# Performance work log

Hardware: AMD Instinct MI355X
Metric: run time of the kernel (lower is better)

## Reference

```python
import jax, jax.numpy as jnp
import numpy as np

N_HEAD = 8
LN_EPS = 1e-5


def _ln(x, g, b):
    m = jnp.mean(x, axis=-1, keepdims=True)
    v = jnp.mean((x - m) ** 2, axis=-1, keepdims=True)
    return (x - m) * jax.lax.rsqrt(v + LN_EPS) * g + b


def setup_inputs() -> dict:
    B, S, IN, D, F, OUT, L = 4, 2048, 3, 512, 2048, 20, 6
    key = jax.random.key(0)
    ks = jax.random.split(key, 22)
    sc = 0.02
    return {
        'src': jax.random.normal(ks[0], (B, S, IN), jnp.float32),
        'W_in': jax.random.normal(ks[1], (IN, D), jnp.float32) * sc,
        'b_in': jnp.zeros((D,), jnp.float32),
        'Wq': jax.random.normal(ks[2], (L, D, D), jnp.float32) * sc,
        'bq': jnp.zeros((L, D), jnp.float32),
        'Wk': jax.random.normal(ks[3], (L, D, D), jnp.float32) * sc,
        'bk': jnp.zeros((L, D), jnp.float32),
        'Wv': jax.random.normal(ks[4], (L, D, D), jnp.float32) * sc,
        'bv': jnp.zeros((L, D), jnp.float32),
        'Wo': jax.random.normal(ks[5], (L, D, D), jnp.float32) * sc,
        'bo': jnp.zeros((L, D), jnp.float32),
        'ln1_g': jnp.ones((L, D), jnp.float32),
        'ln1_b': jnp.zeros((L, D), jnp.float32),
        'W1': jax.random.normal(ks[6], (L, D, F), jnp.float32) * sc,
        'b1': jnp.zeros((L, F), jnp.float32),
        'W2': jax.random.normal(ks[7], (L, F, D), jnp.float32) * sc,
        'b2': jnp.zeros((L, D), jnp.float32),
        'ln2_g': jnp.ones((L, D), jnp.float32),
        'ln2_b': jnp.zeros((L, D), jnp.float32),
        'W_out': jax.random.normal(ks[8], (D, OUT), jnp.float32) * sc,
        'b_out': jnp.zeros((OUT,), jnp.float32),
    }


def reference(src, W_in, b_in, Wq, bq, Wk, bk, Wv, bv, Wo, bo, ln1_g, ln1_b,
              W1, b1, W2, b2, ln2_g, ln2_b, W_out, b_out):
    x = src @ W_in + b_in            # [B, S, D]
    B, S, D = x.shape
    dh = D // N_HEAD
    scale = 1.0 / np.sqrt(dh).astype(np.float32)

    def layer(x, p):
        wq, biq, wk, bik, wv, biv, wo, bio, g1, be1, w1, bi1, w2, bi2, g2, be2 = p
        q = (x @ wq + biq).reshape(B, S, N_HEAD, dh)
        k = (x @ wk + bik).reshape(B, S, N_HEAD, dh)
        v = (x @ wv + biv).reshape(B, S, N_HEAD, dh)
        # flex_attention with score_mod=None == plain scaled dot-product attention
        scores = jnp.einsum('bqhd,bkhd->bhqk', q, k) * scale
        a = jax.nn.softmax(scores, axis=-1)
        o = jnp.einsum('bhqk,bkhd->bqhd', a, v).reshape(B, S, D)
        attn = o @ wo + bio
        h = _ln(x + attn, g1, be1)                       # post-norm (norm_first=False)
        ff = jax.nn.relu(h @ w1 + bi1) @ w2 + bi2
        h = _ln(h + ff, g2, be2)
        return h, None

    x, _ = jax.lax.scan(layer, x, (Wq, bq, Wk, bk, Wv, bv, Wo, bo,
                                   ln1_g, ln1_b, W1, b1, W2, b2, ln2_g, ln2_b))
    return x @ W_out + b_out         # [B, S, OUT]
```

## Files before the change

kernel.cpp:

```cpp
#include <hip/hip_runtime.h>

typedef unsigned short u16;
typedef unsigned int u32;
typedef __bf16 bf16x8 __attribute__((ext_vector_type(8)));
typedef float f32x4 __attribute__((ext_vector_type(4)));
typedef float f32x16 __attribute__((ext_vector_type(16)));

__device__ __forceinline__ u16 f2bf(float f) {
    union { float f; u32 u; } v; v.f = f;
    u32 r = v.u + 0x7FFFu + ((v.u >> 16) & 1u);
    return (u16)(r >> 16);
}

__device__ __forceinline__ u16 bfu(float x) {
    __bf16 b = (__bf16)x;
    union { __bf16 b; u16 u; } c; c.b = b; return c.u;
}

__device__ __forceinline__ void gload16(const u16* g, u16* l) {
    __builtin_amdgcn_global_load_lds((const __attribute__((address_space(1))) void*)g,
                                     (__attribute__((address_space(3))) void*)l, 16, 0, 0);
}

__global__ void wtrans(const float* __restrict__ W, u16* __restrict__ Wt,
                       int K, int N, int rowOff, int dstLd, long long dstStride)
{
    __shared__ float tile[32][33];
    const int l = blockIdx.z;
    const float* Wl = W + (size_t)l * K * N;
    u16* Wtl = Wt + (size_t)l * dstStride;
    const int tx = threadIdx.x, ty = threadIdx.y;
    const int x = blockIdx.x * 32 + tx;
    const int y0 = blockIdx.y * 32;
#pragma unroll
    for (int j = 0; j < 32; j += 8) tile[ty + j][tx] = Wl[(size_t)(y0 + ty + j) * N + x];
    __syncthreads();
    const int n0 = blockIdx.x * 32;
    const int k = y0 + tx;
#pragma unroll
    for (int j = 0; j < 32; j += 8)
        Wtl[(size_t)(rowOff + n0 + ty + j) * dstLd + k] = f2bf(tile[tx][ty + j]);
}

__global__ __launch_bounds__(256) void input_proj(const float* __restrict__ src,
    const float* __restrict__ Wi, const float* __restrict__ bi,
    float* __restrict__ xf, u16* __restrict__ xb)
{
    int idx = blockIdx.x * 256 + threadIdx.x;
    int m = idx >> 9, n = idx & 511;
    float v = bi[n] + src[m * 3] * Wi[n] + src[m * 3 + 1] * Wi[512 + n] + src[m * 3 + 2] * Wi[1024 + n];
    xf[idx] = v;
    xb[idx] = f2bf(v);
}

template<int EPI>
__global__ __launch_bounds__(256) void gemm_bt(
    const u16* __restrict__ A, const u16* __restrict__ Bt,
    const float* __restrict__ bias,
    float* __restrict__ Cf, u16* __restrict__ Cb,
    u16* __restrict__ Qo, u16* __restrict__ Ko, u16* __restrict__ Vo,
    const float* __restrict__ bq, const float* __restrict__ bk, const float* __restrict__ bv,
    int M, int N, int K)
{
    __shared__ u16 As[128 * 32];
    __shared__ u16 Bs[128 * 32];
    const int tid = threadIdx.x;
    const int lane = tid & 63, wid = tid >> 6;
    const int bn = blockIdx.x, bm = blockIdx.y;
    const int row0 = bm * 128, col0 = bn * 128;
    const int srow = lane >> 2, skc = lane & 3;
    const int c0 = wid * 2, c1 = wid * 2 + 1;
    const u16* gA0 = A + (size_t)(row0 + c0 * 16 + srow) * K + skc * 8;
    const u16* gA1 = A + (size_t)(row0 + c1 * 16 + srow) * K + skc * 8;
    const u16* gB0 = Bt + (size_t)(col0 + c0 * 16 + srow) * K + skc * 8;
    const u16* gB1 = Bt + (size_t)(col0 + c1 * 16 + srow) * K + skc * 8;
    u16* lA0 = &As[c0 * 512]; u16* lA1 = &As[c1 * 512];
    u16* lB0 = &Bs[c0 * 512]; u16* lB1 = &Bs[c1 * 512];
    const int wr = (wid >> 1) * 64, wc = (wid & 1) * 64;
    const int cc = lane & 15, qg = lane >> 4;
    const int arow0 = (wr + cc) * 32 + qg * 8;
    const int brow0 = (wc + cc) * 32 + qg * 8;
    f32x4 acc[4][4] = {};
    for (int k0 = 0; k0 < K; k0 += 32) {
        __syncthreads();
        gload16(gA0 + k0, lA0);
        gload16(gA1 + k0, lA1);
        gload16(gB0 + k0, lB0);
        gload16(gB1 + k0, lB1);
        __syncthreads();
        bf16x8 af[4], bfr[4];
#pragma unroll
        for (int i = 0; i < 4; i++) af[i] = *(const bf16x8*)&As[arow0 + i * 512];
#pragma unroll
        for (int i = 0; i < 4; i++) bfr[i] = *(const bf16x8*)&Bs[brow0 + i * 512];
#pragma unroll
        for (int mi = 0; mi < 4; mi++)
#pragma unroll
            for (int ni = 0; ni < 4; ni++)
                acc[mi][ni] = __builtin_amdgcn_mfma_f32_16x16x32_bf16(af[mi], bfr[ni], acc[mi][ni], 0, 0, 0);
    }
    const int q4 = qg * 4;
    if (EPI == 2) {
#pragma unroll
        for (int mi = 0; mi < 4; mi++) {
            int grow = row0 + wr + mi * 16 + q4;
            int btok = grow >> 11, srem = grow & 2047;
#pragma unroll
            for (int ni = 0; ni < 4; ni++) {
                int gcol = col0 + wc + ni * 16 + cc;
                int sec = gcol >> 9, f = gcol & 511;
                int hh = f >> 6, dd = f & 63;
                if (sec == 0) {
                    float bb = bq[f];
                    size_t base = (((size_t)btok * 8 + hh) * 2048 + srem) * 64 + dd;
#pragma unroll
                    for (int i = 0; i < 4; i++) Qo[base + (size_t)i * 64] = f2bf((acc[mi][ni][i] + bb) * 0.18033688f);
                } else if (sec == 1) {
                    float bb = bk[f];
                    size_t base = (((size_t)btok * 8 + hh) * 2048 + srem) * 64 + dd;
#pragma unroll
                    for (int i = 0; i < 4; i++) Ko[base + (size_t)i * 64] = f2bf(acc[mi][ni][i] + bb);
                } else {
                    float bb = bv[f];
                    size_t base = (((size_t)btok * 8 + hh) * 64 + dd) * 2048 + srem;
#pragma unroll
                    for (int i = 0; i < 4; i++) Vo[base + i] = f2bf(acc[mi][ni][i] + bb);
                }
            }
        }
    } else {
#pragma unroll
        for (int mi = 0; mi < 4; mi++) {
            int grow = row0 + wr + mi * 16 + q4;
#pragma unroll
            for (int ni = 0; ni < 4; ni++) {
                int gcol = col0 + wc + ni * 16 + cc;
                float bb = bias[gcol];
#pragma unroll
                for (int i = 0; i < 4; i++) {
                    float v = acc[mi][ni][i] + bb;
                    if (EPI == 0) Cf[(size_t)(grow + i) * N + gcol] = v;
                    else          Cb[(size_t)(grow + i) * N + gcol] = f2bf(v > 0.f ? v : 0.f);
                }
            }
        }
    }
}

__global__ __launch_bounds__(256) void gemm_bt_n64(
    const u16* __restrict__ A, const u16* __restrict__ Bt,
    const float* __restrict__ bias, float* __restrict__ Cf,
    int M, int N, int K)
{
    __shared__ u16 As[128 * 64];
    __shared__ u16 Bs[64 * 64];
    const int tid = threadIdx.x;
    const int lane = tid & 63, wid = tid >> 6;
    const int row0 = blockIdx.y * 128, col0 = blockIdx.x * 64;
    const int wr = (wid >> 1) * 64, wc = (wid & 1) * 32;
    const int cc = lane & 15, qg = lane >> 4;
    f32x4 acc[4][2] = {};
    for (int k0 = 0; k0 < K; k0 += 64) {
        __syncthreads();
#pragma unroll
        for (int j = 0; j < 4; j++) {
            int s = j * 256 + tid;
            int r = s >> 3, g = s & 7;
            gload16(A + (size_t)(row0 + r) * K + k0 + (g ^ (r & 7)) * 8, &As[s * 8]);
        }
#pragma unroll
        for (int j = 0; j < 2; j++) {
            int s = j * 256 + tid;
            int r = s >> 3, g = s & 7;
            gload16(Bt + (size_t)(col0 + r) * K + k0 + (g ^ (r & 7)) * 8, &Bs[s * 8]);
        }
        __syncthreads();
        bf16x8 af[4][2], bfr[2][2];
#pragma unroll
        for (int i = 0; i < 4; i++) {
            int r = wr + i * 16 + cc;
#pragma unroll
            for (int kk = 0; kk < 2; kk++) {
                int g = kk * 4 + qg;
                af[i][kk] = *(const bf16x8*)&As[r * 64 + (g ^ (r & 7)) * 8];
            }
        }
#pragma unroll
        for (int i = 0; i < 2; i++) {
            int r = wc + i * 16 + cc;
#pragma unroll
            for (int kk = 0; kk < 2; kk++) {
                int g = kk * 4 + qg;
                bfr[i][kk] = *(const bf16x8*)&Bs[r * 64 + (g ^ (r & 7)) * 8];
            }
        }
#pragma unroll
        for (int mi = 0; mi < 4; mi++)
#pragma unroll
            for (int ni = 0; ni < 2; ni++) {
                acc[mi][ni] = __builtin_amdgcn_mfma_f32_16x16x32_bf16(af[mi][0], bfr[ni][0], acc[mi][ni], 0, 0, 0);
                acc[mi][ni] = __builtin_amdgcn_mfma_f32_16x16x32_bf16(af[mi][1], bfr[ni][1], acc[mi][ni], 0, 0, 0);
            }
    }
    const int q4 = qg * 4;
#pragma unroll
    for (int mi = 0; mi < 4; mi++) {
        int grow = row0 + wr + mi * 16 + q4;
#pragma unroll
        for (int ni = 0; ni < 2; ni++) {
            int gcol = col0 + wc + ni * 16 + cc;
            float bb = bias[gcol];
#pragma unroll
            for (int i = 0; i < 4; i++)
                Cf[(size_t)(grow + i) * N + gcol] = acc[mi][ni][i] + bb;
        }
    }
}

__global__ __launch_bounds__(128) void flash_attn(
    const u16* __restrict__ Qb, const u16* __restrict__ Kb, const u16* __restrict__ Vt,
    u16* __restrict__ Ob)
{
    __shared__ u16 Ks[2][4096];
    __shared__ u16 Vs[2][4096];
    const int tid = threadIdx.x, lane = tid & 63, w = tid >> 6;
    const int l31 = lane & 31, h = lane >> 5;
    const int bh = blockIdx.x, qt = blockIdx.y;
    const u16* Kg = Kb + (size_t)bh * (2048 * 64);
    const u16* Vg = Vt + (size_t)bh * (64 * 2048);

    bf16x8 qf[4];
    {
        const u16* Qrow = Qb + ((size_t)bh * 2048 + (size_t)qt * 64 + w * 32 + l31) * 64;
#pragma unroll
        for (int f = 0; f < 4; f++) qf[f] = *(const bf16x8*)(Qrow + f * 16 + h * 8);
    }
    f32x16 os0{}, os1{};
    float lsum = 0.f;

    const int sr = tid >> 3, sg = tid & 7;
#pragma unroll
    for (int j = 0; j < 4; j++) {
        int r = j * 16 + sr;
        int gsw = (sg ^ (r & 7)) * 8;
        gload16(Kg + (size_t)r * 64 + gsw, &Ks[0][(j * 128 + w * 64) * 8]);
        gload16(Vg + (size_t)r * 2048 + gsw, &Vs[0][(j * 128 + w * 64) * 8]);
    }
    const int swz = (l31 & 7) << 3;

    for (int kt = 0; kt < 32; kt++) {
        const int cur = kt & 1;
        asm volatile("s_waitcnt vmcnt(0)" ::: "memory");
        __syncthreads();
        if (kt < 31) {
#pragma unroll
            for (int j = 0; j < 4; j++) {
                int r = j * 16 + sr;
                int gsw = (sg ^ (r & 7)) * 8;
                gload16(Kg + (size_t)(kt + 1) * 4096 + (size_t)r * 64 + gsw, &Ks[cur ^ 1][(j * 128 + w * 64) * 8]);
                gload16(Vg + (size_t)r * 2048 + (size_t)(kt + 1) * 64 + gsw, &Vs[cur ^ 1][(j * 128 + w * 64) * 8]);
            }
        }
        f32x16 p0{}, p1{};
        {
            const u16* kb = &Ks[cur][0];
            __builtin_amdgcn_s_setprio(1);
#pragma unroll
            for (int f = 0; f < 4; f++) {
                int colu = (f * 16 + h * 8) ^ swz;
                bf16x8 ka0 = *(const bf16x8*)(kb + l31 * 64 + colu);
                bf16x8 ka1 = *(const bf16x8*)(kb + (32 + l31) * 64 + colu);
                p0 = __builtin_amdgcn_mfma_f32_32x32x16_bf16(ka0, qf[f], p0, 0, 0, 0);
                p1 = __builtin_amdgcn_mfma_f32_32x32x16_bf16(ka1, qf[f], p1, 0, 0, 0);
            }
            __builtin_amdgcn_s_setprio(0);
        }
        float ss[4] = {};
#pragma unroll
        for (int r = 0; r < 16; r++) { float e = __builtin_amdgcn_exp2f(p0[r]); p0[r] = e; ss[r & 3] += e; }
#pragma unroll
        for (int r = 0; r < 16; r++) { float e = __builtin_amdgcn_exp2f(p1[r]); p1[r] = e; ss[r & 3] += e; }
        lsum += (ss[0] + ss[1]) + (ss[2] + ss[3]);
        const u16* vb = &Vs[cur][0];
#pragma unroll
        for (int t = 0; t < 2; t++) {
            u32 pk[8], sw[8];
#pragma unroll
            for (int j = 0; j < 8; j++) {
                float a = t ? p1[2 * j] : p0[2 * j];
                float b = t ? p1[2 * j + 1] : p0[2 * j + 1];
                pk[j] = (u32)bfu(a) | ((u32)bfu(b) << 16);
                sw[j] = __shfl_xor(pk[j], 32);
            }
            union { u32 u[4]; bf16x8 v; } fA, fB;
            fA.u[0] = h ? sw[2] : pk[0];
            fA.u[1] = h ? sw[3] : pk[1];
            fA.u[2] = h ? pk[2] : sw[0];
            fA.u[3] = h ? pk[3] : sw[1];
            fB.u[0] = h ? sw[6] : pk[4];
            fB.u[1] = h ? sw[7] : pk[5];
            fB.u[2] = h ? pk[6] : sw[4];
            fB.u[3] = h ? pk[7] : sw[5];
            __builtin_amdgcn_s_setprio(1);
#pragma unroll
            for (int f = 0; f < 2; f++) {
                bf16x8 pa = f ? fB.v : fA.v;
                int colu = (t * 32 + f * 16 + h * 8) ^ swz;
                bf16x8 v0 = *(const bf16x8*)(vb + l31 * 64 + colu);
                bf16x8 v1 = *(const bf16x8*)(vb + (32 + l31) * 64 + colu);
                os0 = __builtin_amdgcn_mfma_f32_32x32x16_bf16(pa, v0, os0, 0, 0, 0);
                os1 = __builtin_amdgcn_mfma_f32_32x32x16_bf16(pa, v1, os1, 0, 0, 0);
            }
            __builtin_amdgcn_s_setprio(0);
        }
    }
    lsum += __shfl_xor(lsum, 32);
    float rl = 1.f / lsum;
    const int hatt = bh & 7, b_ = bh >> 3;
#pragma unroll
    for (int r = 0; r < 16; r++) {
        int qrow = (r & 3) + 8 * (r >> 2) + 4 * h;
        float rlq = __shfl(rl, qrow);
        int tok = qt * 64 + w * 32 + qrow;
        u16* po = Ob + ((size_t)b_ * 2048 + tok) * 512 + hatt * 64;
        po[l31] = bfu(os0[r] * rlq);
        po[32 + l31] = bfu(os1[r] * rlq);
    }
}

__global__ __launch_bounds__(256) void ln_res(
    const float* __restrict__ X, const float* __restrict__ Y,
    const float* __restrict__ g, const float* __restrict__ bta,
    float* __restrict__ Of, u16* __restrict__ Ob)
{
    const int lane = threadIdx.x & 63;
    const int row = blockIdx.x * 4 + (threadIdx.x >> 6);
    const size_t base = (size_t)row * 512 + lane * 8;
    float4 x0 = *(const float4*)(X + base);
    float4 x1 = *(const float4*)(X + base + 4);
    float4 y0 = *(const float4*)(Y + base);
    float4 y1 = *(const float4*)(Y + base + 4);
    float t[8] = {x0.x + y0.x, x0.y + y0.y, x0.z + y0.z, x0.w + y0.w,
                  x1.x + y1.x, x1.y + y1.y, x1.z + y1.z, x1.w + y1.w};
    float s = 0.f, s2 = 0.f;
#pragma unroll
    for (int j = 0; j < 8; j++) { s += t[j]; s2 += t[j] * t[j]; }
#pragma unroll
    for (int off = 1; off < 64; off <<= 1) { s += __shfl_xor(s, off); s2 += __shfl_xor(s2, off); }
    float mean = s * (1.f / 512.f);
    float var = s2 * (1.f / 512.f) - mean * mean;
    float rs = rsqrtf(var + 1e-5f);
    float4 g0 = *(const float4*)(g + lane * 8);
    float4 g1 = *(const float4*)(g + lane * 8 + 4);
    float4 b0 = *(const float4*)(bta + lane * 8);
    float4 b1 = *(const float4*)(bta + lane * 8 + 4);
    float gg[8] = {g0.x, g0.y, g0.z, g0.w, g1.x, g1.y, g1.z, g1.w};
    float bb[8] = {b0.x, b0.y, b0.z, b0.w, b1.x, b1.y, b1.z, b1.w};
    float o[8];
#pragma unroll
    for (int j = 0; j < 8; j++) o[j] = (t[j] - mean) * rs * gg[j] + bb[j];
    *(float4*)(Of + base) = make_float4(o[0], o[1], o[2], o[3]);
    *(float4*)(Of + base + 4) = make_float4(o[4], o[5], o[6], o[7]);
    u32 p0 = (u32)f2bf(o[0]) | ((u32)f2bf(o[1]) << 16);
    u32 p1 = (u32)f2bf(o[2]) | ((u32)f2bf(o[3]) << 16);
    u32 p2 = (u32)f2bf(o[4]) | ((u32)f2bf(o[5]) << 16);
    u32 p3 = (u32)f2bf(o[6]) | ((u32)f2bf(o[7]) << 16);
    *(uint4*)(Ob + base) = make_uint4(p0, p1, p2, p3);
}

__global__ __launch_bounds__(320) void out_proj(const float* __restrict__ x,
    const float* __restrict__ W, const float* __restrict__ b, float* __restrict__ out)
{
    int t = blockIdx.x * 320 + threadIdx.x;
    int m = t / 20, o = t - m * 20;
    const float* xr = x + (size_t)m * 512;
    float acc = b[o];
#pragma unroll 8
    for (int k = 0; k < 512; k++) acc = fmaf(xr[k], W[k * 20 + o], acc);
    out[(size_t)m * 20 + o] = acc;
}

extern "C" void kernel_launch(void* const* d_in, const int* in_sizes, int n_in,
                              void* d_out, int out_size, void* d_ws, size_t ws_size,
                              hipStream_t stream)
{
    const float* src  = (const float*)d_in[0];
    const float* W_in = (const float*)d_in[1];
    const float* b_in = (const float*)d_in[2];
    const float* Wq   = (const float*)d_in[3];
    const float* bq   = (const float*)d_in[4];
    const float* Wk   = (const float*)d_in[5];
    const float* bk   = (const float*)d_in[6];
    const float* Wv   = (const float*)d_in[7];
    const float* bv   = (const float*)d_in[8];
    const float* Wo   = (const float*)d_in[9];
    const float* bo   = (const float*)d_in[10];
    const float* ln1g = (const float*)d_in[11];
    const float* ln1b = (const float*)d_in[12];
    const float* W1   = (const float*)d_in[13];
    const float* b1   = (const float*)d_in[14];
    const float* W2   = (const float*)d_in[15];
    const float* b2   = (const float*)d_in[16];
    const float* ln2g = (const float*)d_in[17];
    const float* ln2b = (const float*)d_in[18];
    const float* Wout = (const float*)d_in[19];
    const float* bout = (const float*)d_in[20];

    char* ws = (char*)d_ws;
    size_t off = 0;
    auto take = [&](size_t bytes) -> void* {
        off = (off + 255) & ~(size_t)255;
        void* p = ws + off;
        off += bytes;
        return p;
    };
    const size_t TOK = 8192, D = 512;
    u16*   qkvt = (u16*)take(6ull * 1536 * 512 * 2);
    u16*   wot  = (u16*)take(6ull * 512 * 512 * 2);
    u16*   w1t  = (u16*)take(6ull * 2048 * 512 * 2);
    u16*   w2t  = (u16*)take(6ull * 512 * 2048 * 2);
    float* xf   = (float*)take(TOK * D * 4);
    u16*   xb   = (u16*)take(TOK * D * 2);
    u16*   sh4  = (u16*)take(4ull * TOK * D * 2);
    float* scr  = (float*)take(TOK * D * 4);
    float* h1f  = (float*)take(TOK * D * 4);
    u16*   h1b  = (u16*)take(TOK * D * 2);
    if (off > ws_size) return;

    u16* qb  = sh4;
    u16* kb_ = sh4 + TOK * D;
    u16* vtb = sh4 + 2 * TOK * D;
    u16* ob  = sh4 + 3 * TOK * D;
    u16* ffb = sh4;

    dim3 tb(32, 8);
    wtrans<<<dim3(16, 16, 6), tb, 0, stream>>>(Wq, qkvt, 512, 512, 0,    512, 1536ll * 512);
    wtrans<<<dim3(16, 16, 6), tb, 0, stream>>>(Wk, qkvt, 512, 512, 512,  512, 1536ll * 512);
    wtrans<<<dim3(16, 16, 6), tb, 0, stream>>>(Wv, qkvt, 512, 512, 1024, 512, 1536ll * 512);
    wtrans<<<dim3(16, 16, 6), tb, 0, stream>>>(Wo, wot,  512, 512, 0,    512, 512ll * 512);
    wtrans<<<dim3(64, 16, 6), tb, 0, stream>>>(W1, w1t,  512, 2048, 0,   512, 2048ll * 512);
    wtrans<<<dim3(16, 64, 6), tb, 0, stream>>>(W2, w2t,  2048, 512, 0,  2048, 512ll * 2048);

    input_proj<<<16384, 256, 0, stream>>>(src, W_in, b_in, xf, xb);

    for (int l = 0; l < 6; l++) {
        const u16* qkvt_l = qkvt + (size_t)l * 1536 * 512;
        const u16* wot_l  = wot  + (size_t)l * 512 * 512;
        const u16* w1t_l  = w1t  + (size_t)l * 2048 * 512;
        const u16* w2t_l  = w2t  + (size_t)l * 512 * 2048;

        gemm_bt<2><<<dim3(12, 64), 256, 0, stream>>>(xb, qkvt_l, nullptr,
            nullptr, nullptr, qb, kb_, vtb,
            bq + l * 512, bk + l * 512, bv + l * 512, 8192, 1536, 512);

        flash_attn<<<dim3(32, 32), 128, 0, stream>>>(qb, kb_, vtb, ob);

        gemm_bt_n64<<<dim3(8, 64), 256, 0, stream>>>(ob, wot_l, bo + l * 512,
            scr, 8192, 512, 512);

        ln_res<<<2048, 256, 0, stream>>>(xf, scr, ln1g + l * 512, ln1b + l * 512, h1f, h1b);

        gemm_bt<1><<<dim3(16, 64), 256, 0, stream>>>(h1b, w1t_l, b1 + l * 2048,
            nullptr, ffb, nullptr, nullptr, nullptr, nullptr, nullptr, nullptr,
            8192, 2048, 512);

        gemm_bt_n64<<<dim3(8, 64), 256, 0, stream>>>(ffb, w2t_l, b2 + l * 512,
            scr, 8192, 512, 2048);

        ln_res<<<2048, 256, 0, stream>>>(h1f, scr, ln2g + l * 512, ln2b + l * 512, xf, xb);
    }

    out_proj<<<512, 320, 0, stream>>>(xf, Wout, bout, (float*)d_out);
}
```

Measured before the change: 1.222 ms.

## Double GEMM K-tile with swizzled LDS and widen flash-attn blocks to 128 queries

The gemm_bt kernel now loads 64-wide K tiles into LDS with an XOR swizzle and issues two MFMAs per fragment per iteration. This halves the number of barrier pairs and reduces LDS bank conflicts. Flash attention now runs 4 waves per block covering 128 query rows, so each K/V tile loaded into LDS is reused by twice as many queries. In exchange it uses more LDS per GEMM block and launches half as many attention blocks, which may lower occupancy.

```diff
diff --git a/kernel.cpp b/kernel.cpp
--- a/kernel.cpp
+++ b/kernel.cpp
@@ -62,42 +62,52 @@
     const float* __restrict__ bq, const float* __restrict__ bk, const float* __restrict__ bv,
     int M, int N, int K)
 {
-    __shared__ u16 As[128 * 32];
-    __shared__ u16 Bs[128 * 32];
+    __shared__ u16 As[128 * 64];
+    __shared__ u16 Bs[128 * 64];
     const int tid = threadIdx.x;
     const int lane = tid & 63, wid = tid >> 6;
-    const int bn = blockIdx.x, bm = blockIdx.y;
-    const int row0 = bm * 128, col0 = bn * 128;
-    const int srow = lane >> 2, skc = lane & 3;
-    const int c0 = wid * 2, c1 = wid * 2 + 1;
-    const u16* gA0 = A + (size_t)(row0 + c0 * 16 + srow) * K + skc * 8;
-    const u16* gA1 = A + (size_t)(row0 + c1 * 16 + srow) * K + skc * 8;
-    const u16* gB0 = Bt + (size_t)(col0 + c0 * 16 + srow) * K + skc * 8;
-    const u16* gB1 = Bt + (size_t)(col0 + c1 * 16 + srow) * K + skc * 8;
-    u16* lA0 = &As[c0 * 512]; u16* lA1 = &As[c1 * 512];
-    u16* lB0 = &Bs[c0 * 512]; u16* lB1 = &Bs[c1 * 512];
+    const int row0 = blockIdx.y * 128, col0 = blockIdx.x * 128;
     const int wr = (wid >> 1) * 64, wc = (wid & 1) * 64;
     const int cc = lane & 15, qg = lane >> 4;
-    const int arow0 = (wr + cc) * 32 + qg * 8;
-    const int brow0 = (wc + cc) * 32 + qg * 8;
+    const int sr = tid >> 3, sg = tid & 7;
     f32x4 acc[4][4] = {};
-    for (int k0 = 0; k0 < K; k0 += 32) {
+    for (int k0 = 0; k0 < K; k0 += 64) {
         __syncthreads();
-        gload16(gA0 + k0, lA0);
-        gload16(gA1 + k0, lA1);
-        gload16(gB0 + k0, lB0);
-        gload16(gB1 + k0, lB1);
+#pragma unroll
+        for (int j = 0; j < 4; j++) {
+            int r = j * 32 + sr;
+            int gsw = (sg ^ (r & 7)) * 8;
+            gload16(A + (size_t)(row0 + r) * K + k0 + gsw, &As[(j * 256 + tid) * 8]);
+        }
+#pragma unroll
+        for (int j = 0; j < 4; j++) {
+            int r = j * 32 + sr;
+            int gsw = (sg ^ (r & 7)) * 8;
+            gload16(Bt + (size_t)(col0 + r) * K + k0 + gsw, &Bs[(j * 256 + tid) * 8]);
+        }
         __syncthreads();
-        bf16x8 af[4], bfr[4];
-#pragma unroll
-        for (int i = 0; i < 4; i++) af[i] = *(const bf16x8*)&As[arow0 + i * 512];
-#pragma unroll
-        for (int i = 0; i < 4; i++) bfr[i] = *(const bf16x8*)&Bs[brow0 + i * 512];
+        bf16x8 af[4][2], bfr[4][2];
+#pragma unroll
+        for (int i = 0; i < 4; i++) {
+            int r = wr + i * 16 + cc;
+#pragma unroll
+            for (int kk = 0; kk < 2; kk++)
+                af[i][kk] = *(const bf16x8*)&As[r * 64 + ((kk * 4 + qg) ^ (r & 7)) * 8];
+        }
+#pragma unroll
+        for (int i = 0; i < 4; i++) {
+            int r = wc + i * 16 + cc;
+#pragma unroll
+            for (int kk = 0; kk < 2; kk++)
+                bfr[i][kk] = *(const bf16x8*)&Bs[r * 64 + ((kk * 4 + qg) ^ (r & 7)) * 8];
+        }
 #pragma unroll
         for (int mi = 0; mi < 4; mi++)
 #pragma unroll
-            for (int ni = 0; ni < 4; ni++)
-                acc[mi][ni] = __builtin_amdgcn_mfma_f32_16x16x32_bf16(af[mi], bfr[ni], acc[mi][ni], 0, 0, 0);
+            for (int ni = 0; ni < 4; ni++) {
+                acc[mi][ni] = __builtin_amdgcn_mfma_f32_16x16x32_bf16(af[mi][0], bfr[ni][0], acc[mi][ni], 0, 0, 0);
+                acc[mi][ni] = __builtin_amdgcn_mfma_f32_16x16x32_bf16(af[mi][1], bfr[ni][1], acc[mi][ni], 0, 0, 0);
+            }
     }
     const int q4 = qg * 4;
     if (EPI == 2) {
@@ -217,7 +227,7 @@
     }
 }
 
-__global__ __launch_bounds__(128) void flash_attn(
+__global__ __launch_bounds__(256) void flash_attn(
     const u16* __restrict__ Qb, const u16* __restrict__ Kb, const u16* __restrict__ Vt,
     u16* __restrict__ Ob)
 {
@@ -231,20 +241,20 @@
 
     bf16x8 qf[4];
     {
-        const u16* Qrow = Qb + ((size_t)bh * 2048 + (size_t)qt * 64 + w * 32 + l31) * 64;
+        const u16* Qrow = Qb + ((size_t)bh * 2048 + (size_t)qt * 128 + w * 32 + l31) * 64;
 #pragma unroll
         for (int f = 0; f < 4; f++) qf[f] = *(const bf16x8*)(Qrow + f * 16 + h * 8);
     }
     f32x16 os0{}, os1{};
     float lsum = 0.f;
 
-    const int sr = tid >> 3, sg = tid & 7;
-#pragma unroll
-    for (int j = 0; j < 4; j++) {
-        int r = j * 16 + sr;
-        int gsw = (sg ^ (r & 7)) * 8;
-        gload16(Kg + (size_t)r * 64 + gsw, &Ks[0][(j * 128 + w * 64) * 8]);
-        gload16(Vg + (size_t)r * 2048 + gsw, &Vs[0][(j * 128 + w * 64) * 8]);
+    const int r8 = lane >> 3;
+    const int cswz = ((lane & 7) ^ r8) * 8;
+#pragma unroll
+    for (int cc = 0; cc < 2; cc++) {
+        int c = w * 2 + cc;
+        gload16(Kg + (size_t)(c * 8 + r8) * 64 + cswz, &Ks[0][c * 512]);
+        gload16(Vg + (size_t)(c * 8 + r8) * 2048 + cswz, &Vs[0][c * 512]);
     }
     const int swz = (l31 & 7) << 3;
 
@@ -254,11 +264,10 @@
         __syncthreads();
         if (kt < 31) {
 #pragma unroll
-            for (int j = 0; j < 4; j++) {
-                int r = j * 16 + sr;
-                int gsw = (sg ^ (r & 7)) * 8;
-                gload16(Kg + (size_t)(kt + 1) * 4096 + (size_t)r * 64 + gsw, &Ks[cur ^ 1][(j * 128 + w * 64) * 8]);
-                gload16(Vg + (size_t)r * 2048 + (size_t)(kt + 1) * 64 + gsw, &Vs[cur ^ 1][(j * 128 + w * 64) * 8]);
+            for (int cc = 0; cc < 2; cc++) {
+                int c = w * 2 + cc;
+                gload16(Kg + (size_t)(kt + 1) * 4096 + (size_t)(c * 8 + r8) * 64 + cswz, &Ks[cur ^ 1][c * 512]);
+                gload16(Vg + (size_t)(c * 8 + r8) * 2048 + (size_t)(kt + 1) * 64 + cswz, &Vs[cur ^ 1][c * 512]);
             }
         }
         f32x16 p0{}, p1{};
@@ -321,7 +330,7 @@
     for (int r = 0; r < 16; r++) {
         int qrow = (r & 3) + 8 * (r >> 2) + 4 * h;
         float rlq = __shfl(rl, qrow);
-        int tok = qt * 64 + w * 32 + qrow;
+        int tok = qt * 128 + w * 32 + qrow;
         u16* po = Ob + ((size_t)b_ * 2048 + tok) * 512 + hatt * 64;
         po[l31] = bfu(os0[r] * rlq);
         po[32 + l31] = bfu(os1[r] * rlq);
@@ -453,7 +462,7 @@
             nullptr, nullptr, qb, kb_, vtb,
             bq + l * 512, bk + l * 512, bv + l * 512, 8192, 1536, 512);
 
-        flash_attn<<<dim3(32, 32), 128, 0, stream>>>(qb, kb_, vtb, ob);
+        flash_attn<<<dim3(32, 16), 256, 0, stream>>>(qb, kb_, vtb, ob);
 
         gemm_bt_n64<<<dim3(8, 64), 256, 0, stream>>>(ob, wot_l, bo + l * 512,
             scr, 8192, 512, 512);
```

New measurement: 1.140 ms. 6.7% less time.
